# Kernel tuning notes

Hardware: AMD Instinct MI355X
Metric: run time of the kernel (lower is better)

## Reference

```python
import jax, jax.numpy as jnp
import numpy as np

HEAD_DIM = 256
V_DIM = 256
HIDDEN = 1024
SCALE_BASE = 512
GAMMA = 0.96875
BATCH, SEQ = 4, 4096


def _dup_interleave(m):
    # (L, d/2) -> (L, d), duplicating each column consecutively
    return jnp.repeat(m, 2, axis=-1)


def _rotate_every_two(x):
    x1 = x[..., ::2]
    x2 = x[..., 1::2]
    return jnp.stack([-x2, x1], axis=-1).reshape(x.shape)


def _xpos(x, downscale=False):
    # x: (B, L, head_dim); offset=0 path of XPOS.forward
    B, L, Dh = x.shape
    half = Dh // 2
    scale_buf = (jnp.arange(0, Dh, 2, dtype=jnp.float32) + 0.4 * Dh) / (1.4 * Dh)  # (half,)
    pos = jnpp = jnp.arange(L, dtype=jnp.float32)
    scale = scale_buf[None, :] ** (pos / SCALE_BASE)[:, None]  # (L, half)
    inv_freq = 1.0 / (10000.0 ** (jnp.arange(half, dtype=jnp.float32) / half))
    sinusoid = pos[:, None] * inv_freq[None, :]  # (L, half)
    sin, cos = jnp.sin(sinusoid), jnp.cos(sinusoid)
    if downscale:
        scale = 1.0 / scale
    cos_s = _dup_interleave(cos * scale)  # (L, Dh)
    sin_s = _dup_interleave(sin * scale)
    return x * cos_s[None] + _rotate_every_two(x) * sin_s[None]


def _decay_matrix(L):
    n = jnp.arange(L)[:, None]
    m = jnp.arange(L)[None, :]
    mask = n >= m
    expo = jnp.where(mask, n - m, 0).astype(jnp.float32)
    return jnp.where(mask, GAMMA ** expo, 0.0)  # (L, L)


def setup_inputs() -> dict:
    key = jax.random.key(0)
    k1, k2, k3, k4 = jax.random.split(key, 4)
    X = jax.random.normal(k1, (BATCH, SEQ, HIDDEN), dtype=jnp.float32)
    W_Q = jax.random.normal(k2, (HIDDEN, HEAD_DIM), dtype=jnp.float32) / HIDDEN
    W_K = jax.random.normal(k3, (HIDDEN, HEAD_DIM), dtype=jnp.float32) / HIDDEN
    W_V = jax.random.normal(k4, (HIDDEN, V_DIM), dtype=jnp.float32) / HIDDEN
    return {"X": X, "W_Q": W_Q, "W_K": W_K, "W_V": W_V}


def reference(X, W_Q, W_K, W_V):
    L = X.shape[1]
    Q = _xpos(X @ W_Q)                      # (B, L, Dh)
    K = _xpos(X @ W_K, downscale=True)      # (B, L, Dh)
    V = X @ W_V                             # (B, L, Dv)
    D = _decay_matrix(L)                    # (L, L)
    ret = jnp.einsum('bqd,bkd->bqk', Q, K) * D[None]  # (B, L, L)
    return ret @ V                          # (B, L, Dv)
```

## Files before the change

kernel.cpp:

```cpp
#include <hip/hip_runtime.h>
#include <hip/hip_bf16.h>
#include <cstdint>
#include <cstddef>

#define L_SEQ 4096
#define BATCH_N 4
#define HID 1024
#define DH 256
#define LOG2_GAMMA (-0.045803689613124953f)
#define INV_GAMMA32 (2.7620582f)

typedef __attribute__((ext_vector_type(8))) short short8;
typedef __attribute__((ext_vector_type(4))) float floatx4;

__device__ __forceinline__ unsigned short f2bf(float f) {
    union { float f; unsigned int u; } v; v.f = f;
    unsigned int r = (v.u + 0x7FFFu + ((v.u >> 16) & 1u)) >> 16;
    return (unsigned short)r;
}

__device__ __forceinline__ void async_copy16(const unsigned short* gsrc,
                                             unsigned short* lds) {
    __builtin_amdgcn_global_load_lds(
        (const __attribute__((address_space(1))) unsigned int*)gsrc,
        (__attribute__((address_space(3))) unsigned int*)lds, 16, 0, 0);
}

__global__ __launch_bounds__(256) void convert_x_kernel(
    const float* __restrict__ X, unsigned short* __restrict__ Xb)
{
    const int i = (blockIdx.x * 256 + threadIdx.x) * 4;
    const float4 v = *(const float4*)&X[i];
    ushort4 p;
    p.x = f2bf(v.x); p.y = f2bf(v.y); p.z = f2bf(v.z); p.w = f2bf(v.w);
    *(ushort4*)&Xb[i] = p;
}

__global__ __launch_bounds__(256) void xpos_table_kernel(
    float2* __restrict__ tabQ, float2* __restrict__ tabK)
{
    const int gid = blockIdx.x * 256 + threadIdx.x;
    const int i2  = gid >> 12;
    const int pos = gid & (L_SEQ - 1);
    const float e   = (float)pos * (1.0f / 512.0f);
    const float sb  = ((float)(2 * i2) + 102.4f) * (1.0f / 358.4f);
    const float scQ = exp2f(log2f(sb) * e);
    const float scK = 1.0f / scQ;
    const float invf = exp2f(-13.287712379549449f *
                             ((float)i2 * (1.0f / 128.0f)));
    float s, c;
    sincosf((float)pos * invf, &s, &c);
    tabQ[gid] = make_float2(c * scQ, s * scQ);
    tabK[gid] = make_float2(c * scK, s * scK);
}

__global__ __launch_bounds__(256) void transpose_w_kernel(
    const float* __restrict__ WQ, const float* __restrict__ WK,
    const float* __restrict__ WV, unsigned short* __restrict__ Wt)
{
    __shared__ float Ts[64][68];
    const int n0 = blockIdx.x * 64;
    const int k0 = blockIdx.y * 64;
    const int seg = n0 >> 8;
    const float* __restrict__ W = (seg == 0) ? WQ : (seg == 1) ? WK : WV;
    const int nl0 = n0 & 255;

    const int t  = threadIdx.x;
    const int r  = t >> 4;
    const int c4 = (t & 15) * 4;
    #pragma unroll
    for (int i = 0; i < 4; ++i) {
        const int kk = r + i * 16;
        const float4 v = *(const float4*)&W[(size_t)(k0 + kk) * DH + nl0 + c4];
        Ts[c4 + 0][kk] = v.x;
        Ts[c4 + 1][kk] = v.y;
        Ts[c4 + 2][kk] = v.z;
        Ts[c4 + 3][kk] = v.w;
    }
    __syncthreads();
    const int rn = t >> 3;
    const int c8 = (t & 7) * 8;
    #pragma unroll
    for (int i = 0; i < 2; ++i) {
        const int rr = rn + i * 32;
        ushort4 p0, p1;
        p0.x = f2bf(Ts[rr][c8 + 0]); p0.y = f2bf(Ts[rr][c8 + 1]);
        p0.z = f2bf(Ts[rr][c8 + 2]); p0.w = f2bf(Ts[rr][c8 + 3]);
        p1.x = f2bf(Ts[rr][c8 + 4]); p1.y = f2bf(Ts[rr][c8 + 5]);
        p1.z = f2bf(Ts[rr][c8 + 6]); p1.w = f2bf(Ts[rr][c8 + 7]);
        unsigned short* dst = &Wt[(size_t)(n0 + rr) * HID + k0 + c8];
        *(ushort4*)dst       = p0;
        *(ushort4*)(dst + 4) = p1;
    }
}

__global__ __launch_bounds__(256) void gemm_qkv_kernel(
    const unsigned short* __restrict__ Wt,
    const unsigned short* __restrict__ Xb,
    const float2* __restrict__ tabQ,
    const float2* __restrict__ tabK,
    unsigned short* __restrict__ Qo,
    unsigned short* __restrict__ Ko,
    unsigned short* __restrict__ VtG)
{
    __shared__ unsigned short Wa[3][128][32];
    __shared__ unsigned short Xs[3][128][32];

    const int dblk = blockIdx.x;
    const int xcd  = dblk & 7;
    const int sq   = dblk >> 3;
    const int by   = xcd * 16 + sq / 6;
    const int bx   = sq % 6;

    const int n0 = bx * 128;
    const int p0 = by * 128;
    const int t    = threadIdx.x;
    const int w    = t >> 6;
    const int lane = t & 63;
    const int quad = lane >> 4;
    const int l16  = lane & 15;
    const int wn   = (w & 1) * 64;
    const int wp   = (w >> 1) * 64;

    const int srow = w * 32 + (lane >> 2);
    const int scol = (lane & 3) * 8;

    floatx4 acc[4][4];
    #pragma unroll
    for (int i = 0; i < 4; ++i)
        #pragma unroll
        for (int j = 0; j < 4; ++j) acc[i][j] = (floatx4){0.f, 0.f, 0.f, 0.f};

    const int NT = HID / 32;

    auto stage = [&](int buf, int kt) {
        const int k0 = kt * 32;
        #pragma unroll
        for (int is = 0; is < 2; ++is) {
            const unsigned short* ga =
                &Wt[(size_t)(n0 + srow + is * 16) * HID + k0 + scol];
            const unsigned short* gb =
                &Xb[(size_t)(p0 + srow + is * 16) * HID + k0 + scol];
            async_copy16(ga, &Wa[buf][w * 32 + is * 16][0]);
            async_copy16(gb, &Xs[buf][w * 32 + is * 16][0]);
        }
    };

    stage(0, 0);
    stage(1, 1);

    for (int kt = 0; kt < NT; ++kt) {
        const int buf = kt % 3;
        if (kt + 1 < NT)
            asm volatile("s_waitcnt vmcnt(4)" ::: "memory");
        else
            asm volatile("s_waitcnt vmcnt(0)" ::: "memory");
        __builtin_amdgcn_s_barrier();

        if (kt + 2 < NT) stage((kt + 2) % 3, kt + 2);

        short8 af[4], bfv[4];
        #pragma unroll
        for (int nt = 0; nt < 4; ++nt)
            af[nt] = *(const short8*)&Wa[buf][wn + nt * 16 + l16][quad * 8];
        #pragma unroll
        for (int pt = 0; pt < 4; ++pt)
            bfv[pt] = *(const short8*)&Xs[buf][wp + pt * 16 + l16][quad * 8];
        #pragma unroll
        for (int nt = 0; nt < 4; ++nt)
            #pragma unroll
            for (int pt = 0; pt < 4; ++pt)
                acc[nt][pt] = __builtin_amdgcn_mfma_f32_16x16x32_bf16(
                    af[nt], bfv[pt], acc[nt][pt], 0, 0, 0);
    }

    const int seg = n0 >> 8;
    const float2* __restrict__ tab = (seg == 1) ? tabK : tabQ;
    #pragma unroll
    for (int nt = 0; nt < 4; ++nt) {
        const int nfeat = n0 + wn + nt * 16 + quad * 4;
        const int d0 = nfeat & 255;
        #pragma unroll
        for (int pt = 0; pt < 4; ++pt) {
            const int pg  = p0 + wp + pt * 16 + l16;
            const int b   = pg >> 12;
            const int pos = pg & (L_SEQ - 1);
            if (seg == 2) {
                #pragma unroll
                for (int g = 0; g < 4; ++g)
                    VtG[(((size_t)(b * 256 + d0 + g)) << 12) + pos] =
                        f2bf(acc[nt][pt][g]);
            } else {
                float res[4];
                #pragma unroll
                for (int h = 0; h < 4; h += 2) {
                    const int i2 = (d0 + h) >> 1;
                    const float2 tc = tab[(i2 << 12) + pos];
                    const float cs = tc.x, ss = tc.y;
                    const float xe = acc[nt][pt][h], xo = acc[nt][pt][h + 1];
                    res[h]     = xe * cs - xo * ss;
                    res[h + 1] = xo * cs + xe * ss;
                }
                ushort4 pk;
                pk.x = f2bf(res[0]); pk.y = f2bf(res[1]);
                pk.z = f2bf(res[2]); pk.w = f2bf(res[3]);
                unsigned short* orow =
                    ((seg == 0) ? Qo : Ko) + (size_t)pg * DH + d0;
                *(ushort4*)orow = pk;
            }
        }
    }
}

__global__ __launch_bounds__(256) void retention_kernel(
    const unsigned short* __restrict__ Q,
    const unsigned short* __restrict__ K,
    const unsigned short* __restrict__ VtG,
    float* __restrict__ O)
{
    __shared__ short Ks[32][264];
    __shared__ short Vt[256][40];

    const int dblk = blockIdx.x;
    const int xcd  = dblk & 7;
    const int sq   = dblk >> 3;
    const int qt   = xcd * 8 + (sq & 7);
    const int b    = (sq >> 3) & 3;
    const int z    = sq >> 5;

    const int t  = threadIdx.x;
    const int q0 = qt * 64;

    const int w    = t >> 6;
    const int lane = t & 63;
    const int quad = lane >> 4;
    const int l16  = lane & 15;
    const int w16  = w * 16;

    const size_t rbase = (size_t)b * L_SEQ * DH;
    const size_t vbase = ((size_t)b * DH) << 12;

    int kst = q0 - 512; if (kst < 0) kst = 0;
    const int half32 = ((q0 + 64 - kst) >> 6) << 5;
    const int kbeg = kst + (z ? half32 : 0);
    const int kfin = z ? (q0 + 64) : (kst + half32);

    short8 qf[8];
    {
        const unsigned short* qsrc = Q + rbase + (size_t)(q0 + w16 + l16) * DH;
        #pragma unroll
        for (int dd = 0; dd < 8; ++dd)
            qf[dd] = *(const short8*)&qsrc[dd * 32 + quad * 8];
    }

    int   dint[8];
    float dec[8];
    #pragma unroll
    for (int nt = 0; nt < 2; ++nt)
        #pragma unroll
        for (int g = 0; g < 4; ++g) {
            const int idx = nt * 4 + g;
            dint[idx] = (q0 + w16 + l16) - (kbeg + nt * 16 + quad * 4 + g);
            dec[idx]  = exp2f((float)dint[idx] * LOG2_GAMMA);
        }

    floatx4 o[16];
    #pragma unroll
    for (int f = 0; f < 16; ++f) o[f] = (floatx4){0.f, 0.f, 0.f, 0.f};

    const int s0   = (quad & 1) * 2;
    const int idxA = (s0 * 16 + l16) * 4;
    const int idxB = idxA + 64;
    const bool lo  = (quad < 2);

    for (int k0 = kbeg; k0 < kfin; k0 += 32) {
        __syncthreads();
        {
            const unsigned short* src = K + rbase + (size_t)k0 * DH;
            #pragma unroll
            for (int i = 0; i < 4; ++i) {
                const int row = i * 8 + (t >> 5);
                const int col = (t & 31) * 8;
                *(uint4*)&Ks[row][col] = *(const uint4*)&src[row * DH + col];
            }
        }
        {
            const int c0   = t >> 2;
            const int koff = (t & 3) * 8;
            #pragma unroll
            for (int i = 0; i < 4; ++i) {
                const int c = c0 + 64 * i;
                *(uint4*)&Vt[c][koff] =
                    *(const uint4*)&VtG[vbase + ((size_t)c << 12) + k0 + koff];
            }
        }
        __syncthreads();

        floatx4 sA0 = (floatx4){0.f, 0.f, 0.f, 0.f};
        floatx4 sA1 = (floatx4){0.f, 0.f, 0.f, 0.f};
        floatx4 sB0 = (floatx4){0.f, 0.f, 0.f, 0.f};
        floatx4 sB1 = (floatx4){0.f, 0.f, 0.f, 0.f};
        #pragma unroll
        for (int dd = 0; dd < 4; ++dd) {
            const short8 k0f = *(const short8*)&Ks[l16][dd * 32 + quad * 8];
            const short8 k1f = *(const short8*)&Ks[16 + l16][dd * 32 + quad * 8];
            const short8 k0g = *(const short8*)&Ks[l16][(dd + 4) * 32 + quad * 8];
            const short8 k1g = *(const short8*)&Ks[16 + l16][(dd + 4) * 32 + quad * 8];
            sA0 = __builtin_amdgcn_mfma_f32_16x16x32_bf16(k0f, qf[dd], sA0, 0, 0, 0);
            sA1 = __builtin_amdgcn_mfma_f32_16x16x32_bf16(k1f, qf[dd], sA1, 0, 0, 0);
            sB0 = __builtin_amdgcn_mfma_f32_16x16x32_bf16(k0g, qf[dd + 4], sB0, 0, 0, 0);
            sB1 = __builtin_amdgcn_mfma_f32_16x16x32_bf16(k1g, qf[dd + 4], sB1, 0, 0, 0);
        }
        const floatx4 sv0 = sA0 + sB0;
        const floatx4 sv1 = sA1 + sB1;

        unsigned int pk01[2], pk23[2];
        #pragma unroll
        for (int nt = 0; nt < 2; ++nt) {
            const floatx4 sv = nt ? sv1 : sv0;
            float pv[4];
            #pragma unroll
            for (int g = 0; g < 4; ++g) {
                const int idx = nt * 4 + g;
                pv[g] = (dint[idx] >= 0) ? sv[g] * dec[idx] : 0.0f;
            }
            pk01[nt] = ((unsigned int)f2bf(pv[1]) << 16) | (unsigned int)f2bf(pv[0]);
            pk23[nt] = ((unsigned int)f2bf(pv[3]) << 16) | (unsigned int)f2bf(pv[2]);
        }
        #pragma unroll
        for (int i = 0; i < 8; ++i) { dint[i] -= 32; dec[i] *= INV_GAMMA32; }

        const int a01_0 = __builtin_amdgcn_ds_bpermute(idxA, (int)pk01[0]);
        const int a01_1 = __builtin_amdgcn_ds_bpermute(idxA, (int)pk01[1]);
        const int a23_0 = __builtin_amdgcn_ds_bpermute(idxA, (int)pk23[0]);
        const int a23_1 = __builtin_amdgcn_ds_bpermute(idxA, (int)pk23[1]);
        const int b01_0 = __builtin_amdgcn_ds_bpermute(idxB, (int)pk01[0]);
        const int b01_1 = __builtin_amdgcn_ds_bpermute(idxB, (int)pk01[1]);
        const int b23_0 = __builtin_amdgcn_ds_bpermute(idxB, (int)pk23[0]);
        const int b23_1 = __builtin_amdgcn_ds_bpermute(idxB, (int)pk23[1]);
        union { int u[4]; short8 s8; } af;
        af.u[0] = lo ? a01_0 : a01_1;
        af.u[1] = lo ? a23_0 : a23_1;
        af.u[2] = lo ? b01_0 : b01_1;
        af.u[3] = lo ? b23_0 : b23_1;

        #pragma unroll
        for (int f = 0; f < 16; ++f) {
            const short8 bfr = *(const short8*)&Vt[f * 16 + l16][quad * 8];
            o[f] = __builtin_amdgcn_mfma_f32_16x16x32_bf16(af.s8, bfr, o[f], 0, 0, 0);
        }
    }

    #pragma unroll
    for (int f = 0; f < 16; ++f) {
        #pragma unroll
        for (int g = 0; g < 4; ++g) {
            const int qpos = q0 + w16 + quad * 4 + g;
            atomicAdd(&O[rbase + (size_t)qpos * DH + f * 16 + l16], o[f][g]);
        }
    }
}

extern "C" void kernel_launch(void* const* d_in, const int* in_sizes, int n_in,
                              void* d_out, int out_size, void* d_ws, size_t ws_size,
                              hipStream_t stream)
{
    const float* X  = (const float*)d_in[0];
    const float* WQ = (const float*)d_in[1];
    const float* WK = (const float*)d_in[2];
    const float* WV = (const float*)d_in[3];
    float* out = (float*)d_out;

    const size_t per = (size_t)BATCH_N * L_SEQ * DH;
    unsigned short* Qw  = (unsigned short*)d_ws;
    unsigned short* Kw  = Qw + per;
    unsigned short* Vtw = Kw + per;
    unsigned short* Xbw = Vtw + per;
    unsigned short* Wtw = Xbw + (size_t)16384 * HID;
    float2* tabQ = (float2*)(Wtw + 786432);
    float2* tabK = tabQ + (size_t)128 * L_SEQ;

    hipMemsetAsync(out, 0, per * sizeof(float), stream);

    xpos_table_kernel<<<2048, 256, 0, stream>>>(tabQ, tabK);
    convert_x_kernel<<<16384, 256, 0, stream>>>(X, Xbw);
    transpose_w_kernel<<<dim3(12, 16), 256, 0, stream>>>(WQ, WK, WV, Wtw);

    gemm_qkv_kernel<<<768, 256, 0, stream>>>(Wtw, Xbw, tabQ, tabK, Qw, Kw, Vtw);

    retention_kernel<<<512, 256, 0, stream>>>(Qw, Kw, Vtw, out);
}
```

Before: 203.0 us.

## Merge prep kernels and memset into one launch; reorder GEMM LDS staging layout

Folds the X conversion, xpos table build, weight transpose and output zeroing into a single block-dispatched prep kernel, removing three launches and a memset. It also changes the QKV GEMM's async global-to-LDS staging so each 16-row group is stored k-quad-major, with fragment reads adjusted to match. The new layout is meant to make LDS fragment reads conflict-free and contiguous per quad. The fused kernel carries the transpose path's shared-memory footprint in every block, which may lower occupancy for the simple conversion blocks.

```diff
diff --git a/kernel.cpp b/kernel.cpp
--- a/kernel.cpp
+++ b/kernel.cpp
@@ -26,71 +26,77 @@
         (__attribute__((address_space(3))) unsigned int*)lds, 16, 0, 0);
 }
 
-__global__ __launch_bounds__(256) void convert_x_kernel(
-    const float* __restrict__ X, unsigned short* __restrict__ Xb)
-{
-    const int i = (blockIdx.x * 256 + threadIdx.x) * 4;
-    const float4 v = *(const float4*)&X[i];
-    ushort4 p;
-    p.x = f2bf(v.x); p.y = f2bf(v.y); p.z = f2bf(v.z); p.w = f2bf(v.w);
-    *(ushort4*)&Xb[i] = p;
-}
-
-__global__ __launch_bounds__(256) void xpos_table_kernel(
-    float2* __restrict__ tabQ, float2* __restrict__ tabK)
-{
-    const int gid = blockIdx.x * 256 + threadIdx.x;
-    const int i2  = gid >> 12;
-    const int pos = gid & (L_SEQ - 1);
-    const float e   = (float)pos * (1.0f / 512.0f);
-    const float sb  = ((float)(2 * i2) + 102.4f) * (1.0f / 358.4f);
-    const float scQ = exp2f(log2f(sb) * e);
-    const float scK = 1.0f / scQ;
-    const float invf = exp2f(-13.287712379549449f *
-                             ((float)i2 * (1.0f / 128.0f)));
-    float s, c;
-    sincosf((float)pos * invf, &s, &c);
-    tabQ[gid] = make_float2(c * scQ, s * scQ);
-    tabK[gid] = make_float2(c * scK, s * scK);
-}
-
-__global__ __launch_bounds__(256) void transpose_w_kernel(
+__global__ __launch_bounds__(256) void prep_kernel(
+    const float* __restrict__ X, unsigned short* __restrict__ Xb,
+    float2* __restrict__ tabQ, float2* __restrict__ tabK,
     const float* __restrict__ WQ, const float* __restrict__ WK,
-    const float* __restrict__ WV, unsigned short* __restrict__ Wt)
+    const float* __restrict__ WV, unsigned short* __restrict__ Wt,
+    float* __restrict__ O)
 {
     __shared__ float Ts[64][68];
-    const int n0 = blockIdx.x * 64;
-    const int k0 = blockIdx.y * 64;
-    const int seg = n0 >> 8;
-    const float* __restrict__ W = (seg == 0) ? WQ : (seg == 1) ? WK : WV;
-    const int nl0 = n0 & 255;
-
-    const int t  = threadIdx.x;
-    const int r  = t >> 4;
-    const int c4 = (t & 15) * 4;
-    #pragma unroll
-    for (int i = 0; i < 4; ++i) {
-        const int kk = r + i * 16;
-        const float4 v = *(const float4*)&W[(size_t)(k0 + kk) * DH + nl0 + c4];
-        Ts[c4 + 0][kk] = v.x;
-        Ts[c4 + 1][kk] = v.y;
-        Ts[c4 + 2][kk] = v.z;
-        Ts[c4 + 3][kk] = v.w;
-    }
-    __syncthreads();
-    const int rn = t >> 3;
-    const int c8 = (t & 7) * 8;
-    #pragma unroll
-    for (int i = 0; i < 2; ++i) {
-        const int rr = rn + i * 32;
-        ushort4 p0, p1;
-        p0.x = f2bf(Ts[rr][c8 + 0]); p0.y = f2bf(Ts[rr][c8 + 1]);
-        p0.z = f2bf(Ts[rr][c8 + 2]); p0.w = f2bf(Ts[rr][c8 + 3]);
-        p1.x = f2bf(Ts[rr][c8 + 4]); p1.y = f2bf(Ts[rr][c8 + 5]);
-        p1.z = f2bf(Ts[rr][c8 + 6]); p1.w = f2bf(Ts[rr][c8 + 7]);
-        unsigned short* dst = &Wt[(size_t)(n0 + rr) * HID + k0 + c8];
-        *(ushort4*)dst       = p0;
-        *(ushort4*)(dst + 4) = p1;
+    const int bid = blockIdx.x;
+    const int t   = threadIdx.x;
+
+    if (bid < 16384) {
+        const int i = (bid * 256 + t) * 4;
+        const float4 v = *(const float4*)&X[i];
+        ushort4 p;
+        p.x = f2bf(v.x); p.y = f2bf(v.y); p.z = f2bf(v.z); p.w = f2bf(v.w);
+        *(ushort4*)&Xb[i] = p;
+    } else if (bid < 18432) {
+        const int gid = (bid - 16384) * 256 + t;
+        const int i2  = gid >> 12;
+        const int pos = gid & (L_SEQ - 1);
+        const float e   = (float)pos * (1.0f / 512.0f);
+        const float sb  = ((float)(2 * i2) + 102.4f) * (1.0f / 358.4f);
+        const float scQ = exp2f(log2f(sb) * e);
+        const float scK = 1.0f / scQ;
+        const float invf = exp2f(-13.287712379549449f *
+                                 ((float)i2 * (1.0f / 128.0f)));
+        float s, c;
+        sincosf((float)pos * invf, &s, &c);
+        tabQ[gid] = make_float2(c * scQ, s * scQ);
+        tabK[gid] = make_float2(c * scK, s * scK);
+    } else if (bid < 18624) {
+        const int idx = bid - 18432;
+        const int n0 = (idx % 12) * 64;
+        const int k0 = (idx / 12) * 64;
+        const int seg = n0 >> 8;
+        const float* __restrict__ W = (seg == 0) ? WQ : (seg == 1) ? WK : WV;
+        const int nl0 = n0 & 255;
+
+        const int r  = t >> 4;
+        const int c4 = (t & 15) * 4;
+        #pragma unroll
+        for (int i = 0; i < 4; ++i) {
+            const int kk = r + i * 16;
+            const float4 v = *(const float4*)&W[(size_t)(k0 + kk) * DH + nl0 + c4];
+            Ts[c4 + 0][kk] = v.x;
+            Ts[c4 + 1][kk] = v.y;
+            Ts[c4 + 2][kk] = v.z;
+            Ts[c4 + 3][kk] = v.w;
+        }
+        __syncthreads();
+        const int rn = t >> 3;
+        const int c8 = (t & 7) * 8;
+        #pragma unroll
+        for (int i = 0; i < 2; ++i) {
+            const int rr = rn + i * 32;
+            ushort4 p0, p1;
+            p0.x = f2bf(Ts[rr][c8 + 0]); p0.y = f2bf(Ts[rr][c8 + 1]);
+            p0.z = f2bf(Ts[rr][c8 + 2]); p0.w = f2bf(Ts[rr][c8 + 3]);
+            p1.x = f2bf(Ts[rr][c8 + 4]); p1.y = f2bf(Ts[rr][c8 + 5]);
+            p1.z = f2bf(Ts[rr][c8 + 6]); p1.w = f2bf(Ts[rr][c8 + 7]);
+            unsigned short* dst = &Wt[(size_t)(n0 + rr) * HID + k0 + c8];
+            *(ushort4*)dst       = p0;
+            *(ushort4*)(dst + 4) = p1;
+        }
+    } else {
+        const int gid = (bid - 18624) * 256 + t;
+        float4 z = (float4){0.f, 0.f, 0.f, 0.f};
+        float4* dst = (float4*)O + (size_t)gid * 8;
+        #pragma unroll
+        for (int i = 0; i < 8; ++i) dst[i] = z;
     }
 }
 
@@ -122,8 +128,8 @@
     const int wn   = (w & 1) * 64;
     const int wp   = (w >> 1) * 64;
 
-    const int srow = w * 32 + (lane >> 2);
-    const int scol = (lane & 3) * 8;
+    const int r16 = lane & 15;
+    const int kq8 = (lane >> 4) * 8;
 
     floatx4 acc[4][4];
     #pragma unroll
@@ -138,9 +144,9 @@
         #pragma unroll
         for (int is = 0; is < 2; ++is) {
             const unsigned short* ga =
-                &Wt[(size_t)(n0 + srow + is * 16) * HID + k0 + scol];
+                &Wt[(size_t)(n0 + w * 32 + is * 16 + r16) * HID + k0 + kq8];
             const unsigned short* gb =
-                &Xb[(size_t)(p0 + srow + is * 16) * HID + k0 + scol];
+                &Xb[(size_t)(p0 + w * 32 + is * 16 + r16) * HID + k0 + kq8];
             async_copy16(ga, &Wa[buf][w * 32 + is * 16][0]);
             async_copy16(gb, &Xs[buf][w * 32 + is * 16][0]);
         }
@@ -159,13 +165,17 @@
 
         if (kt + 2 < NT) stage((kt + 2) % 3, kt + 2);
 
+        const char* wbp = (const char*)&Wa[buf][0][0];
+        const char* xbp = (const char*)&Xs[buf][0][0];
         short8 af[4], bfv[4];
         #pragma unroll
         for (int nt = 0; nt < 4; ++nt)
-            af[nt] = *(const short8*)&Wa[buf][wn + nt * 16 + l16][quad * 8];
+            af[nt] = *(const short8*)(wbp + ((w & 1) * 4 + nt) * 1024 +
+                                      quad * 256 + l16 * 16);
         #pragma unroll
         for (int pt = 0; pt < 4; ++pt)
-            bfv[pt] = *(const short8*)&Xs[buf][wp + pt * 16 + l16][quad * 8];
+            bfv[pt] = *(const short8*)(xbp + ((w >> 1) * 4 + pt) * 1024 +
+                                       quad * 256 + l16 * 16);
         #pragma unroll
         for (int nt = 0; nt < 4; ++nt)
             #pragma unroll
@@ -380,11 +390,8 @@
     float2* tabQ = (float2*)(Wtw + 786432);
     float2* tabK = tabQ + (size_t)128 * L_SEQ;
 
-    hipMemsetAsync(out, 0, per * sizeof(float), stream);
-
-    xpos_table_kernel<<<2048, 256, 0, stream>>>(tabQ, tabK);
-    convert_x_kernel<<<16384, 256, 0, stream>>>(X, Xbw);
-    transpose_w_kernel<<<dim3(12, 16), 256, 0, stream>>>(WQ, WK, WV, Wtw);
+    prep_kernel<<<19136, 256, 0, stream>>>(X, Xbw, tabQ, tabK,
+                                           WQ, WK, WV, Wtw, out);
 
     gemm_qkv_kernel<<<768, 256, 0, stream>>>(Wtw, Xbw, tabQ, tabK, Qw, Kw, Vtw);
 
```

Result: slower. 213.3 us (+5.1%).
